# Optimization experiments

Hardware: AMD Instinct MI355X
Metric: run time of the kernel (lower is better)

Reference implementation:

```python
import jax, jax.numpy as jnp
import numpy as np

ALPHA = 0.2
NEG = -9e15
EPS = 1e-5


def _gat(h, adj, W, a, out_features):
    # h: [B,N,Fin], adj: [B,N,N], W: [Fin,Fout], a: [2*Fout,1]
    Wh = jnp.matmul(h, W)                      # [B,N,Fout]
    Wh1 = jnp.matmul(Wh, a[:out_features])     # [B,N,1]
    Wh2 = jnp.matmul(Wh, a[out_features:])     # [B,N,1]
    e = Wh1 + jnp.swapaxes(Wh2, 1, 2)          # [B,N,N]
    e = jax.nn.leaky_relu(e, negative_slope=ALPHA)
    scores = jnp.where(adj > 0, e, NEG)
    att = jax.nn.softmax(scores, axis=1)       # NOTE: dim=1 as in source
    return jnp.matmul(att, Wh)                 # [B,N,Fout]


def _layernorm(x, g, b):
    mu = jnp.mean(x, axis=-1, keepdims=True)
    var = jnp.var(x, axis=-1, keepdims=True)
    return (x - mu) * jax.lax.rsqrt(var + EPS) * g + b


def setup_inputs() -> dict:
    key = jax.random.key(0)
    ks = jax.random.split(key, 8)
    B, N, F, H = 2, 4096, 256, 1024
    x = jax.random.normal(ks[0], (B, N, F), dtype=jnp.float32)
    adj = jax.random.randint(ks[1], (B, N, N), 0, 2, dtype=jnp.int32)
    def xavier(k, shape):
        fan_in, fan_out = shape[0], shape[1]
        lim = np.sqrt(6.0 / (fan_in + fan_out))
        return jax.random.uniform(k, shape, jnp.float32, -lim, lim)
    return {
        "x": x,
        "adj": adj,
        "W1": xavier(ks[2], (F, F)),
        "a1": xavier(ks[3], (2 * F, 1)),
        "W2": xavier(ks[4], (F, F)),
        "a2": xavier(ks[5], (2 * F, 1)),
        "w_ff1": xavier(ks[6], (F, H)) ,
        "b_ff1": jnp.zeros((H,), jnp.float32),
        "w_ff2": xavier(ks[7], (H, F)),
        "b_ff2": jnp.zeros((F,), jnp.float32),
        "g_ln1": jnp.ones((F,), jnp.float32),
        "b_ln1": jnp.zeros((F,), jnp.float32),
        "g_ln2": jnp.ones((F,), jnp.float32),
        "b_ln2": jnp.zeros((F,), jnp.float32),
    }


def reference(x, adj, W1, a1, W2, a2, w_ff1, b_ff1, w_ff2, b_ff2,
              g_ln1, b_ln1, g_ln2, b_ln2):
    Fout = W1.shape[1]
    residual = x
    # dropout is a no-op in eval mode
    h = _gat(x, adj, W1, a1, Fout)          # single head -> cat is identity
    h = _gat(h, adj, W2, a2, W2.shape[1])
    h = _layernorm(residual + h, g_ln1, b_ln1)
    residual2 = h
    ff = jnp.matmul(jax.nn.relu(jnp.matmul(h, w_ff1) + b_ff1), w_ff2) + b_ff2
    return _layernorm(residual2 + ff, g_ln2, b_ln2)
```

## Files before the change

### kernel.cpp

```cpp
#include <hip/hip_runtime.h>
#include <math.h>

#define ALPHA 0.2f
#define NEGV  -9e15f
#define EPSV  1e-5f

constexpr int B_ = 2, N_ = 4096, F_ = 256, H_ = 1024;
constexpr int SPLIT_ = 16;
constexpr int SPLITJ_ = 4;

typedef __attribute__((ext_vector_type(4))) float f32x4;
typedef __attribute__((ext_vector_type(8))) short s16x8;

__device__ __forceinline__ unsigned short f2bf(float f) {
    unsigned u = __builtin_bit_cast(unsigned, f);
    u += 0x7fffu + ((u >> 16) & 1u);
    return (unsigned short)(u >> 16);
}

__global__ __launch_bounds__(256) void zero_kernel(float* __restrict__ p)
{
    const int i = (blockIdx.x * 256 + threadIdx.x) * 4;
    *(float4*)&p[i] = make_float4(0.f, 0.f, 0.f, 0.f);
}

__global__ __launch_bounds__(256) void transp_all_kernel(
    const float* __restrict__ W1, const float* __restrict__ W2,
    const float* __restrict__ F1s, const float* __restrict__ F2s,
    unsigned short* __restrict__ D1, unsigned short* __restrict__ D2,
    unsigned short* __restrict__ D3, unsigned short* __restrict__ D4)
{
    const int mi = blockIdx.z;
    const float* src; unsigned short* dst; int R, Cc;
    if (mi == 0)      { src = W1;  dst = D1; R = 256;  Cc = 256; }
    else if (mi == 1) { src = W2;  dst = D2; R = 256;  Cc = 256; }
    else if (mi == 2) { src = F1s; dst = D3; R = 256;  Cc = 1024; }
    else              { src = F2s; dst = D4; R = 1024; Cc = 256; }
    const int r0 = blockIdx.x * 64, c0 = blockIdx.y * 64;
    if (r0 >= R || c0 >= Cc) return;

    __shared__ float T[64][65];
    const int t = threadIdx.x;
    #pragma unroll
    for (int s = 0; s < 4; ++s) {
        const int rr = s * 16 + (t >> 4);
        const int cq = t & 15;
        const float4 v = *(const float4*)&src[(size_t)(r0 + rr) * Cc + c0 + cq * 4];
        T[rr][cq * 4 + 0] = v.x; T[rr][cq * 4 + 1] = v.y;
        T[rr][cq * 4 + 2] = v.z; T[rr][cq * 4 + 3] = v.w;
    }
    __syncthreads();
    #pragma unroll
    for (int s = 0; s < 4; ++s) {
        const int cr = s * 16 + (t >> 4);
        const int rq = t & 15;
        ushort4 o;
        o.x = f2bf(T[rq * 4 + 0][cr]);
        o.y = f2bf(T[rq * 4 + 1][cr]);
        o.z = f2bf(T[rq * 4 + 2][cr]);
        o.w = f2bf(T[rq * 4 + 3][cr]);
        *(ushort4*)&dst[(size_t)(c0 + cr) * R + r0 + rq * 4] = o;
    }
}

__global__ __launch_bounds__(256) void gemm128_kernel(
    const void* __restrict__ Ap, const unsigned short* __restrict__ Wt,
    const float* __restrict__ bias, void* __restrict__ Cp,
    unsigned short* __restrict__ Tout, const float* __restrict__ wha,
    float* __restrict__ Wh1, float* __restrict__ Wh2,
    int Nc, int K, int relu, int a_bf16, int c_mode)
{
    __shared__ unsigned short As[128 * 72];
    __shared__ unsigned short Bs[128 * 72];
    const int t = threadIdx.x;
    const int w = t >> 6, l = t & 63;
    const int quad = l >> 4, l15 = l & 15;
    const int wr = w & 1, wc = w >> 1;
    const int row0 = blockIdx.y * 128, col0 = blockIdx.x * 128;
    const int sr = t >> 1;
    const int sk = (t & 1) * 32;

    f32x4 acc[4][4];
    #pragma unroll
    for (int it = 0; it < 4; ++it)
        #pragma unroll
        for (int ft = 0; ft < 4; ++ft) acc[it][ft] = (f32x4)(0.f);

    for (int k0 = 0; k0 < K; k0 += 64) {
        if (a_bf16) {
            const unsigned short* ap =
                (const unsigned short*)Ap + (size_t)(row0 + sr) * K + k0 + sk;
            #pragma unroll
            for (int u = 0; u < 4; ++u)
                *(s16x8*)&As[sr * 72 + sk + u * 8] = *(const s16x8*)(ap + u * 8);
        } else {
            const float* ap = (const float*)Ap + (size_t)(row0 + sr) * K + k0 + sk;
            #pragma unroll
            for (int u = 0; u < 8; ++u) {
                const float4 v = *(const float4*)(ap + u * 4);
                ushort4 o;
                o.x = f2bf(v.x); o.y = f2bf(v.y); o.z = f2bf(v.z); o.w = f2bf(v.w);
                *(ushort4*)&As[sr * 72 + sk + u * 4] = o;
            }
        }
        {
            const unsigned short* bp = Wt + (size_t)(col0 + sr) * K + k0 + sk;
            #pragma unroll
            for (int u = 0; u < 4; ++u)
                *(s16x8*)&Bs[sr * 72 + sk + u * 8] = *(const s16x8*)(bp + u * 8);
        }
        __syncthreads();
        #pragma unroll
        for (int ks = 0; ks < 64; ks += 32) {
            s16x8 af[4], bf[4];
            #pragma unroll
            for (int it = 0; it < 4; ++it)
                af[it] = *(const s16x8*)&As[(wr * 64 + it * 16 + l15) * 72 + ks + quad * 8];
            #pragma unroll
            for (int ft = 0; ft < 4; ++ft)
                bf[ft] = *(const s16x8*)&Bs[(wc * 64 + ft * 16 + l15) * 72 + ks + quad * 8];
            #pragma unroll
            for (int ft = 0; ft < 4; ++ft)
                #pragma unroll
                for (int it = 0; it < 4; ++it)
                    acc[it][ft] = __builtin_amdgcn_mfma_f32_16x16x32_bf16(
                        af[it], bf[ft], acc[it][ft], 0, 0, 0);
        }
        __syncthreads();
    }

    if (c_mode) {
        #pragma unroll
        for (int ft = 0; ft < 4; ++ft) {
            const int col = col0 + wc * 64 + ft * 16 + l15;
            const float bv = bias ? bias[col] : 0.f;
            #pragma unroll
            for (int it = 0; it < 4; ++it) {
                const int rbase = row0 + wr * 64 + it * 16 + quad * 4;
                #pragma unroll
                for (int rr = 0; rr < 4; ++rr) {
                    float v = acc[it][ft][rr] + bv;
                    if (relu) v = fmaxf(v, 0.f);
                    if (c_mode == 2)
                        ((unsigned short*)Cp)[(size_t)(rbase + rr) * Nc + col] = f2bf(v);
                    else
                        ((float*)Cp)[(size_t)(rbase + rr) * Nc + col] = v;
                }
            }
        }
    }

    if (Tout) {
        const int bb = row0 >> 12;
        #pragma unroll
        for (int ft = 0; ft < 4; ++ft) {
            const int col = col0 + wc * 64 + ft * 16 + l15;
            #pragma unroll
            for (int it = 0; it < 4; ++it) {
                const int ibase = (row0 & (N_ - 1)) + wr * 64 + it * 16 + quad * 4;
                ushort4 o;
                o.x = f2bf(acc[it][ft][0]); o.y = f2bf(acc[it][ft][1]);
                o.z = f2bf(acc[it][ft][2]); o.w = f2bf(acc[it][ft][3]);
                *(ushort4*)&Tout[((size_t)bb * F_ + col) * N_ + ibase] = o;
            }
        }
    }

    if (wha) {
        float a1v[4], a2v[4];
        #pragma unroll
        for (int ft = 0; ft < 4; ++ft) {
            const int col = col0 + wc * 64 + ft * 16 + l15;
            a1v[ft] = wha[col];
            a2v[ft] = wha[F_ + col];
        }
        #pragma unroll
        for (int it = 0; it < 4; ++it)
            #pragma unroll
            for (int rr = 0; rr < 4; ++rr) {
                float s1 = 0.f, s2 = 0.f;
                #pragma unroll
                for (int ft = 0; ft < 4; ++ft) {
                    s1 += acc[it][ft][rr] * a1v[ft];
                    s2 += acc[it][ft][rr] * a2v[ft];
                }
                #pragma unroll
                for (int mkk = 1; mkk < 16; mkk <<= 1) {
                    s1 += __shfl_xor(s1, mkk);
                    s2 += __shfl_xor(s2, mkk);
                }
                if (l15 == 0) {
                    const int row = row0 + wr * 64 + it * 16 + quad * 4 + rr;
                    atomicAdd(&Wh1[row], s1);
                    atomicAdd(&Wh2[row], s2);
                }
            }
    }
}

__global__ __launch_bounds__(256) void gemm64_kernel(
    const void* __restrict__ Ap, const unsigned short* __restrict__ Wt,
    const float* __restrict__ bias, void* __restrict__ Cp,
    unsigned short* __restrict__ Tout, const float* __restrict__ wha,
    float* __restrict__ Wh1, float* __restrict__ Wh2,
    int Nc, int K, int relu, int a_bf16, int c_mode)
{
    __shared__ unsigned short As[64 * 72];
    __shared__ unsigned short Bs[128 * 72];
    const int t = threadIdx.x;
    const int w = t >> 6, l = t & 63;
    const int quad = l >> 4, l15 = l & 15;
    const int row0 = blockIdx.y * 64, col0 = blockIdx.x * 128;
    const int sra = t >> 2;
    const int ska = (t & 3) * 16;
    const int srb = t >> 1;
    const int skb = (t & 1) * 32;

    f32x4 acc[4][2];
    #pragma unroll
    for (int it = 0; it < 4; ++it)
        #pragma unroll
        for (int ft = 0; ft < 2; ++ft) acc[it][ft] = (f32x4)(0.f);

    for (int k0 = 0; k0 < K; k0 += 64) {
        if (a_bf16) {
            const unsigned short* ap =
                (const unsigned short*)Ap + (size_t)(row0 + sra) * K + k0 + ska;
            *(s16x8*)&As[sra * 72 + ska]     = *(const s16x8*)ap;
            *(s16x8*)&As[sra * 72 + ska + 8] = *(const s16x8*)(ap + 8);
        } else {
            const float* ap = (const float*)Ap + (size_t)(row0 + sra) * K + k0 + ska;
            #pragma unroll
            for (int u = 0; u < 4; ++u) {
                const float4 v = *(const float4*)(ap + u * 4);
                ushort4 o;
                o.x = f2bf(v.x); o.y = f2bf(v.y); o.z = f2bf(v.z); o.w = f2bf(v.w);
                *(ushort4*)&As[sra * 72 + ska + u * 4] = o;
            }
        }
        {
            const unsigned short* bp = Wt + (size_t)(col0 + srb) * K + k0 + skb;
            #pragma unroll
            for (int u = 0; u < 4; ++u)
                *(s16x8*)&Bs[srb * 72 + skb + u * 8] = *(const s16x8*)(bp + u * 8);
        }
        __syncthreads();
        #pragma unroll
        for (int ks = 0; ks < 64; ks += 32) {
            s16x8 af[4], bf[2];
            #pragma unroll
            for (int it = 0; it < 4; ++it)
                af[it] = *(const s16x8*)&As[(it * 16 + l15) * 72 + ks + quad * 8];
            #pragma unroll
            for (int ft = 0; ft < 2; ++ft)
                bf[ft] = *(const s16x8*)&Bs[(w * 32 + ft * 16 + l15) * 72 + ks + quad * 8];
            #pragma unroll
            for (int ft = 0; ft < 2; ++ft)
                #pragma unroll
                for (int it = 0; it < 4; ++it)
                    acc[it][ft] = __builtin_amdgcn_mfma_f32_16x16x32_bf16(
                        af[it], bf[ft], acc[it][ft], 0, 0, 0);
        }
        __syncthreads();
    }

    if (c_mode) {
        #pragma unroll
        for (int ft = 0; ft < 2; ++ft) {
            const int col = col0 + w * 32 + ft * 16 + l15;
            const float bv = bias ? bias[col] : 0.f;
            #pragma unroll
            for (int it = 0; it < 4; ++it) {
                const int rbase = row0 + it * 16 + quad * 4;
                #pragma unroll
                for (int rr = 0; rr < 4; ++rr) {
                    float v = acc[it][ft][rr] + bv;
                    if (relu) v = fmaxf(v, 0.f);
                    if (c_mode == 2)
                        ((unsigned short*)Cp)[(size_t)(rbase + rr) * Nc + col] = f2bf(v);
                    else
                        ((float*)Cp)[(size_t)(rbase + rr) * Nc + col] = v;
                }
            }
        }
    }

    if (Tout) {
        const int bb = row0 >> 12;
        #pragma unroll
        for (int ft = 0; ft < 2; ++ft) {
            const int col = col0 + w * 32 + ft * 16 + l15;
            #pragma unroll
            for (int it = 0; it < 4; ++it) {
                const int ibase = (row0 & (N_ - 1)) + it * 16 + quad * 4;
                ushort4 o;
                o.x = f2bf(acc[it][ft][0]); o.y = f2bf(acc[it][ft][1]);
                o.z = f2bf(acc[it][ft][2]); o.w = f2bf(acc[it][ft][3]);
                *(ushort4*)&Tout[((size_t)bb * F_ + col) * N_ + ibase] = o;
            }
        }
    }

    if (wha) {
        float a1v[2], a2v[2];
        #pragma unroll
        for (int ft = 0; ft < 2; ++ft) {
            const int col = col0 + w * 32 + ft * 16 + l15;
            a1v[ft] = wha[col];
            a2v[ft] = wha[F_ + col];
        }
        #pragma unroll
        for (int it = 0; it < 4; ++it)
            #pragma unroll
            for (int rr = 0; rr < 4; ++rr) {
                float s1 = acc[it][0][rr] * a1v[0] + acc[it][1][rr] * a1v[1];
                float s2 = acc[it][0][rr] * a2v[0] + acc[it][1][rr] * a2v[1];
                #pragma unroll
                for (int mkk = 1; mkk < 16; mkk <<= 1) {
                    s1 += __shfl_xor(s1, mkk);
                    s2 += __shfl_xor(s2, mkk);
                }
                if (l15 == 0) {
                    const int row = row0 + it * 16 + quad * 4 + rr;
                    atomicAdd(&Wh1[row], s1);
                    atomicAdd(&Wh2[row], s2);
                }
            }
    }
}

__global__ __launch_bounds__(256) void colstats_adj_kernel(
    const int* __restrict__ adj, unsigned long long* __restrict__ maskOut,
    const float* __restrict__ Wh1, const float* __restrict__ Wh2,
    float* __restrict__ pM, float* __restrict__ pS)
{
    const int t = threadIdx.x;
    const int j = blockIdx.x * 256 + t;
    const int sp = blockIdx.y;
    const int b = blockIdx.z;
    const int i0 = sp * (N_ / SPLIT_);
    const int w = t >> 6, l = t & 63;
    const float w2 = Wh2[b * N_ + j];
    const float* __restrict__ w1p = Wh1 + b * N_ + i0;
    const int* __restrict__ ap = adj + ((size_t)b * N_ + i0) * N_ + j;

    float m = -3.4e38f, s = 0.f;
    for (int c = 0; c < N_ / SPLIT_; c += 8) {
        int v[8];
        #pragma unroll
        for (int u = 0; u < 8; ++u) v[u] = ap[(size_t)(c + u) * N_];
        float x[8];
        #pragma unroll
        for (int u = 0; u < 8; ++u) {
            const bool act = v[u] > 0;
            const unsigned long long bm = __ballot(act);
            if (l == 0)
                maskOut[((size_t)b * N_ + i0 + c + u) * (N_ / 64) + blockIdx.x * 4 + w] = bm;
            const float e0 = w1p[c + u] + w2;
            const float e = fmaxf(e0, ALPHA * e0);
            x[u] = act ? e : NEGV;
        }
        const float cm = fmaxf(fmaxf(fmaxf(x[0], x[1]), fmaxf(x[2], x[3])),
                               fmaxf(fmaxf(x[4], x[5]), fmaxf(x[6], x[7])));
        const float nm = fmaxf(m, cm);
        float cs = 0.f;
        #pragma unroll
        for (int u = 0; u < 8; ++u) cs += __expf(x[u] - nm);
        s = s * __expf(m - nm) + cs;
        m = nm;
    }
    pM[((size_t)b * SPLIT_ + sp) * N_ + j] = m;
    pS[((size_t)b * SPLIT_ + sp) * N_ + j] = s;
}

__global__ __launch_bounds__(256) void colstats3_kernel(
    const unsigned long long* __restrict__ mask,
    const float* __restrict__ Wh1, const float* __restrict__ Wh2,
    float* __restrict__ pM, float* __restrict__ pS)
{
    const int t = threadIdx.x;
    const int j = blockIdx.x * 256 + t;
    const int sp = blockIdx.y;
    const int b = blockIdx.z;
    const int i0 = sp * (N_ / SPLIT_);
    const int w = t >> 6;
    const int jbit = t & 63;
    const float w2 = Wh2[b * N_ + j];
    const unsigned long long* __restrict__ mbase =
        mask + ((size_t)b * N_ + i0) * (N_ / 64) + blockIdx.x * 4 + w;
    const float* __restrict__ w1p = Wh1 + b * N_ + i0;

    float m = -3.4e38f, s = 0.f;
    for (int c = 0; c < N_ / SPLIT_; c += 8) {
        float x[8];
        #pragma unroll
        for (int u = 0; u < 8; ++u) {
            const unsigned long long mw = mbase[(size_t)(c + u) * (N_ / 64)];
            const float e0 = w1p[c + u] + w2;
            const float e = fmaxf(e0, ALPHA * e0);
            x[u] = ((mw >> jbit) & 1ull) ? e : NEGV;
        }
        const float cm = fmaxf(fmaxf(fmaxf(x[0], x[1]), fmaxf(x[2], x[3])),
                               fmaxf(fmaxf(x[4], x[5]), fmaxf(x[6], x[7])));
        const float nm = fmaxf(m, cm);
        float cs = 0.f;
        #pragma unroll
        for (int u = 0; u < 8; ++u) cs += __expf(x[u] - nm);
        s = s * __expf(m - nm) + cs;
        m = nm;
    }
    pM[((size_t)b * SPLIT_ + sp) * N_ + j] = m;
    pS[((size_t)b * SPLIT_ + sp) * N_ + j] = s;
}

__global__ __launch_bounds__(256) void colfin2_kernel(
    const float* __restrict__ pM, const float* __restrict__ pS,
    float* __restrict__ Mo)
{
    const int j = blockIdx.x * 256 + threadIdx.x;
    const int b = blockIdx.y;
    float m = -3.4e38f;
    #pragma unroll
    for (int s = 0; s < SPLIT_; ++s)
        m = fmaxf(m, pM[((size_t)b * SPLIT_ + s) * N_ + j]);
    float sum = 0.f;
    #pragma unroll
    for (int s = 0; s < SPLIT_; ++s)
        sum += pS[((size_t)b * SPLIT_ + s) * N_ + j] *
               __expf(pM[((size_t)b * SPLIT_ + s) * N_ + j] - m);
    Mo[b * N_ + j] = m + logf(sum);
}

__global__ __launch_bounds__(256, 2) void att_mfma4_kernel(
    const unsigned short* __restrict__ mask16, const unsigned short* __restrict__ Wht,
    const float* __restrict__ Wh1, const float* __restrict__ Wh2,
    const float* __restrict__ Mo, float* __restrict__ part)
{
    __shared__ unsigned short Ps[2][64 * 72];
    __shared__ float w2s[1024];
    __shared__ float mos[1024];

    const int t = threadIdx.x;
    const int w = t >> 6, l = t & 63;
    const int quad = l >> 4, l15 = l & 15;

    const int lin = blockIdx.x + (blockIdx.y << 6) + (blockIdx.z << 8);
    const int xcd = lin & 7;
    const int b = xcd >> 2;
    const int sp = xcd & 3;
    const int i0 = (lin >> 3) << 6;
    const int jbase = sp * (N_ / SPLITJ_);

    const int pi = t >> 2;
    const int pj4 = t & 3;
    const float w1i = Wh1[b * N_ + i0 + pi];
    const unsigned short* __restrict__ mrow =
        mask16 + ((size_t)b * N_ + i0 + pi) * (N_ / 16) + pj4;
    const unsigned short* __restrict__ WhtB = Wht + (size_t)b * F_ * N_;

    {
        const float4 a = *(const float4*)&Wh2[b * N_ + jbase + t * 4];
        const float4 c = *(const float4*)&Mo[b * N_ + jbase + t * 4];
        *(float4*)&w2s[t * 4] = a;
        *(float4*)&mos[t * 4] = c;
    }

    f32x4 acc[4][4];
    #pragma unroll
    for (int it = 0; it < 4; ++it)
        #pragma unroll
        for (int ft = 0; ft < 4; ++ft) acc[it][ft] = (f32x4)(0.f);

    const unsigned short* __restrict__ bbase =
        WhtB + (size_t)(w * 64 + l15) * N_ + jbase + quad * 8;

    s16x8 bA[8], bB[8];

    auto prefB = [&](int itr2, s16x8* dst) {
        const unsigned short* nb = bbase + itr2 * 64;
        #pragma unroll
        for (int ft = 0; ft < 4; ++ft)
            #pragma unroll
            for (int kk = 0; kk < 2; ++kk)
                dst[ft * 2 + kk] = *(const s16x8*)&nb[(size_t)ft * 16 * N_ + kk * 32];
    };

    auto computeP = [&](int itr2, unsigned short* psdst) {
        const int jl = itr2 * 64 + pj4 * 16;
        const unsigned mb = mrow[(jbase >> 4) + itr2 * 4];
        s16x8 o0, o1;
        #pragma unroll
        for (int u4 = 0; u4 < 4; ++u4) {
            const float4 w2v = *(const float4*)&w2s[jl + u4 * 4];
            const float4 mov = *(const float4*)&mos[jl + u4 * 4];
            #pragma unroll
            for (int u = 0; u < 4; ++u) {
                const float xw = w1i + (&w2v.x)[u];
                const float e = fmaxf(xw, ALPHA * xw);
                const float x2 = ((mb >> (u4 * 4 + u)) & 1u) ? e : NEGV;
                const short pv = (short)f2bf(__expf(x2 - (&mov.x)[u]));
                if (u4 < 2) o0[u4 * 4 + u] = pv;
                else        o1[(u4 - 2) * 4 + u] = pv;
            }
        }
        *(s16x8*)&psdst[pi * 72 + pj4 * 16]     = o0;
        *(s16x8*)&psdst[pi * 72 + pj4 * 16 + 8] = o1;
    };

    auto mfmaStep = [&](const unsigned short* ps, const s16x8* breg) {
        #pragma unroll
        for (int ksidx = 0; ksidx < 2; ++ksidx) {
            s16x8 af[4];
            #pragma unroll
            for (int it = 0; it < 4; ++it)
                af[it] = *(const s16x8*)&ps[(it * 16 + l15) * 72 + ksidx * 32 + quad * 8];
            #pragma unroll
            for (int ft = 0; ft < 4; ++ft)
                #pragma unroll
                for (int it = 0; it < 4; ++it)
                    acc[it][ft] = __builtin_amdgcn_mfma_f32_16x16x32_bf16(
                        af[it], breg[ft * 2 + ksidx], acc[it][ft], 0, 0, 0);
        }
    };

    prefB(0, bA);
    __syncthreads();
    computeP(0, &Ps[0][0]);
    __syncthreads();

    constexpr int NITER = (N_ / SPLITJ_) / 64;
    for (int itr = 0; itr < NITER; itr += 2) {
        prefB(itr + 1, bB);
        computeP(itr + 1, &Ps[1][0]);
        mfmaStep(&Ps[0][0], bA);
        __syncthreads();
        if (itr + 2 < NITER) {
            prefB(itr + 2, bA);
            computeP(itr + 2, &Ps[0][0]);
        }
        mfmaStep(&Ps[1][0], bB);
        __syncthreads();
    }

    float* __restrict__ pout = part + ((size_t)sp * B_ + b) * N_ * F_;
    #pragma unroll
    for (int it = 0; it < 4; ++it)
        #pragma unroll
        for (int ft = 0; ft < 4; ++ft) {
            const int col = w * 64 + ft * 16 + l15;
            #pragma unroll
            for (int rr = 0; rr < 4; ++rr) {
                const int row = i0 + it * 16 + quad * 4 + rr;
                pout[(size_t)row * F_ + col] = acc[it][ft][rr];
            }
        }
}

__global__ __launch_bounds__(256) void reduce4b_kernel(
    const float* __restrict__ p, unsigned short* __restrict__ outb)
{
    const size_t i = ((size_t)blockIdx.x * 256 + threadIdx.x) * 4;
    const size_t S = (size_t)B_ * N_ * F_;
    const float4 a = *(const float4*)&p[i];
    const float4 b = *(const float4*)&p[i + S];
    const float4 c = *(const float4*)&p[i + 2 * S];
    const float4 d = *(const float4*)&p[i + 3 * S];
    ushort4 o;
    o.x = f2bf(a.x + b.x + c.x + d.x);
    o.y = f2bf(a.y + b.y + c.y + d.y);
    o.z = f2bf(a.z + b.z + c.z + d.z);
    o.w = f2bf(a.w + b.w + c.w + d.w);
    *(ushort4*)&outb[i] = o;
}

__global__ __launch_bounds__(256) void addln4_kernel(
    const float* __restrict__ X, const float* __restrict__ p,
    const float* __restrict__ g, const float* __restrict__ bta,
    float* __restrict__ outf, unsigned short* __restrict__ outb)
{
    const int row = blockIdx.x;
    const int t = threadIdx.x;
    const size_t idx = (size_t)row * F_ + t;
    const size_t S = (size_t)B_ * N_ * F_;
    const float v = X[idx] + p[idx] + p[idx + S] + p[idx + 2 * S] + p[idx + 3 * S];
    float s1 = v, s2 = v * v;
    #pragma unroll
    for (int off = 32; off > 0; off >>= 1) {
        s1 += __shfl_down(s1, off);
        s2 += __shfl_down(s2, off);
    }
    __shared__ float r1[4], r2[4];
    __shared__ float mu_s, rs_s;
    const int wid = t >> 6, lane = t & 63;
    if (lane == 0) { r1[wid] = s1; r2[wid] = s2; }
    __syncthreads();
    if (t == 0) {
        const float a = r1[0] + r1[1] + r1[2] + r1[3];
        const float q = r2[0] + r2[1] + r2[2] + r2[3];
        const float mu = a * (1.f / F_);
        const float var = q * (1.f / F_) - mu * mu;
        mu_s = mu;
        rs_s = rsqrtf(var + EPSV);
    }
    __syncthreads();
    const float r = (v - mu_s) * rs_s * g[t] + bta[t];
    outf[idx] = r;
    outb[idx] = f2bf(r);
}

__global__ __launch_bounds__(256) void addln_kernel(
    const float* __restrict__ X, const float* __restrict__ Y,
    const float* __restrict__ g, const float* __restrict__ bta,
    float* __restrict__ out)
{
    const int row = blockIdx.x;
    const int t = threadIdx.x;
    const size_t idx = (size_t)row * F_ + t;
    const float v = X[idx] + Y[idx];
    float s1 = v, s2 = v * v;
    #pragma unroll
    for (int off = 32; off > 0; off >>= 1) {
        s1 += __shfl_down(s1, off);
        s2 += __shfl_down(s2, off);
    }
    __shared__ float r1[4], r2[4];
    __shared__ float mu_s, rs_s;
    const int wid = t >> 6, lane = t & 63;
    if (lane == 0) { r1[wid] = s1; r2[wid] = s2; }
    __syncthreads();
    if (t == 0) {
        const float a = r1[0] + r1[1] + r1[2] + r1[3];
        const float q = r2[0] + r2[1] + r2[2] + r2[3];
        const float mu = a * (1.f / F_);
        const float var = q * (1.f / F_) - mu * mu;
        mu_s = mu;
        rs_s = rsqrtf(var + EPSV);
    }
    __syncthreads();
    out[idx] = (v - mu_s) * rs_s * g[t] + bta[t];
}

extern "C" void kernel_launch(void* const* d_in, const int* in_sizes, int n_in,
                              void* d_out, int out_size, void* d_ws, size_t ws_size,
                              hipStream_t stream)
{
    const float* x     = (const float*)d_in[0];
    const int*   adj   = (const int*)d_in[1];
    const float* W1    = (const float*)d_in[2];
    const float* a1    = (const float*)d_in[3];
    const float* W2    = (const float*)d_in[4];
    const float* a2    = (const float*)d_in[5];
    const float* w_ff1 = (const float*)d_in[6];
    const float* b_ff1 = (const float*)d_in[7];
    const float* w_ff2 = (const float*)d_in[8];
    const float* b_ff2 = (const float*)d_in[9];
    const float* g_ln1 = (const float*)d_in[10];
    const float* b_ln1 = (const float*)d_in[11];
    const float* g_ln2 = (const float*)d_in[12];
    const float* b_ln2 = (const float*)d_in[13];
    float* out = (float*)d_out;

    const int Rtot = B_ * N_;
    char* wsb = (char*)d_ws;
    float* part  = (float*)wsb;
    float* ln1   = (float*)(wsb + 33554432);
    float* ffout = (float*)(wsb + 41943040);
    unsigned short* mid  = (unsigned short*)(wsb + 50331648);
    unsigned short* ln1b = (unsigned short*)(wsb + 67108864);
    unsigned short* g1b  = (unsigned short*)(wsb + 71303168);
    unsigned short* Wht  = (unsigned short*)(wsb + 75497472);
    unsigned long long* mask = (unsigned long long*)(wsb + 79691776);
    unsigned short* mask16 = (unsigned short*)mask;
    unsigned short* Wt1  = (unsigned short*)(wsb + 83886080);
    unsigned short* Wt2  = Wt1 + 65536;
    unsigned short* Wtf1 = Wt2 + 65536;
    unsigned short* Wtf2 = Wtf1 + 262144;
    float* WhA1 = (float*)(wsb + 85196800);
    float* WhA2 = WhA1 + 8192;
    float* WhB1 = WhA2 + 8192;
    float* WhB2 = WhB1 + 8192;
    float* Mo   = (float*)(wsb + 85327872);
    float* pM   = (float*)(wsb + 85360640);
    float* pS   = (float*)(wsb + 85884928);

    const dim3 statsG(N_ / 256, SPLIT_, B_);
    const dim3 finG(N_ / 256, B_);
    const dim3 attG(N_ / 64, SPLITJ_, B_);

    zero_kernel<<<32, 256, 0, stream>>>(WhA1);
    transp_all_kernel<<<dim3(16, 16, 4), 256, 0, stream>>>(
        W1, W2, w_ff1, w_ff2, Wt1, Wt2, Wtf1, Wtf2);

    gemm64_kernel<<<dim3(2, 128), 256, 0, stream>>>(
        x, Wt1, nullptr, nullptr, Wht, a1, WhA1, WhA2, F_, F_, 0, 0, 0);
    colstats_adj_kernel<<<statsG, 256, 0, stream>>>(adj, mask, WhA1, WhA2, pM, pS);
    colfin2_kernel<<<finG, 256, 0, stream>>>(pM, pS, Mo);
    att_mfma4_kernel<<<attG, 256, 0, stream>>>(mask16, Wht, WhA1, WhA2, Mo, part);
    reduce4b_kernel<<<2048, 256, 0, stream>>>(part, g1b);

    gemm64_kernel<<<dim3(2, 128), 256, 0, stream>>>(
        g1b, Wt2, nullptr, nullptr, Wht, a2, WhB1, WhB2, F_, F_, 0, 1, 0);
    colstats3_kernel<<<statsG, 256, 0, stream>>>(mask, WhB1, WhB2, pM, pS);
    colfin2_kernel<<<finG, 256, 0, stream>>>(pM, pS, Mo);
    att_mfma4_kernel<<<attG, 256, 0, stream>>>(mask16, Wht, WhB1, WhB2, Mo, part);

    addln4_kernel<<<Rtot, 256, 0, stream>>>(x, part, g_ln1, b_ln1, ln1, ln1b);

    gemm128_kernel<<<dim3(8, 64), 256, 0, stream>>>(
        ln1b, Wtf1, b_ff1, mid, nullptr, nullptr, nullptr, nullptr, H_, F_, 1, 1, 2);
    gemm64_kernel<<<dim3(2, 128), 256, 0, stream>>>(
        mid, Wtf2, b_ff2, ffout, nullptr, nullptr, nullptr, nullptr, F_, H_, 0, 1, 1);

    addln_kernel<<<Rtot, 256, 0, stream>>>(ln1, ffout, g_ln2, b_ln2, out);
}
```

Measured before the change: 424.0 us.

## Remove split-K in attention matmul, use 32-row tiles with 512 threads

```diff
diff --git a/kernel.cpp b/kernel.cpp
--- a/kernel.cpp
+++ b/kernel.cpp
@@ -7,7 +7,6 @@
 
 constexpr int B_ = 2, N_ = 4096, F_ = 256, H_ = 1024;
 constexpr int SPLIT_ = 16;
-constexpr int SPLITJ_ = 4;
 
 typedef __attribute__((ext_vector_type(4))) float f32x4;
 typedef __attribute__((ext_vector_type(8))) short s16x8;
@@ -431,93 +430,91 @@
     Mo[b * N_ + j] = m + logf(sum);
 }
 
-__global__ __launch_bounds__(256, 2) void att_mfma4_kernel(
+__global__ __launch_bounds__(512) void att_mfma5_kernel(
     const unsigned short* __restrict__ mask16, const unsigned short* __restrict__ Wht,
     const float* __restrict__ Wh1, const float* __restrict__ Wh2,
-    const float* __restrict__ Mo, float* __restrict__ part)
-{
-    __shared__ unsigned short Ps[2][64 * 72];
-    __shared__ float w2s[1024];
-    __shared__ float mos[1024];
+    const float* __restrict__ Mo, unsigned short* __restrict__ outb,
+    float* __restrict__ outf)
+{
+    __shared__ unsigned short Ps[2][32 * 72];
+    __shared__ float w2s[N_];
+    __shared__ float mos[N_];
 
     const int t = threadIdx.x;
     const int w = t >> 6, l = t & 63;
     const int quad = l >> 4, l15 = l & 15;
 
-    const int lin = blockIdx.x + (blockIdx.y << 6) + (blockIdx.z << 8);
+    const int lin = blockIdx.x;
     const int xcd = lin & 7;
     const int b = xcd >> 2;
-    const int sp = xcd & 3;
-    const int i0 = (lin >> 3) << 6;
-    const int jbase = sp * (N_ / SPLITJ_);
-
-    const int pi = t >> 2;
-    const int pj4 = t & 3;
+    const int tile = (lin >> 3) * 4 + (xcd & 3);
+    const int i0 = tile * 32;
+
+    const int pi = t >> 4;
+    const int pj = t & 15;
     const float w1i = Wh1[b * N_ + i0 + pi];
     const unsigned short* __restrict__ mrow =
-        mask16 + ((size_t)b * N_ + i0 + pi) * (N_ / 16) + pj4;
+        mask16 + ((size_t)b * N_ + i0 + pi) * (N_ / 16);
     const unsigned short* __restrict__ WhtB = Wht + (size_t)b * F_ * N_;
 
     {
-        const float4 a = *(const float4*)&Wh2[b * N_ + jbase + t * 4];
-        const float4 c = *(const float4*)&Mo[b * N_ + jbase + t * 4];
-        *(float4*)&w2s[t * 4] = a;
-        *(float4*)&mos[t * 4] = c;
-    }
-
-    f32x4 acc[4][4];
-    #pragma unroll
-    for (int it = 0; it < 4; ++it)
-        #pragma unroll
-        for (int ft = 0; ft < 4; ++ft) acc[it][ft] = (f32x4)(0.f);
+        const float4 a0 = *(const float4*)&Wh2[b * N_ + t * 8];
+        const float4 a1 = *(const float4*)&Wh2[b * N_ + t * 8 + 4];
+        const float4 c0 = *(const float4*)&Mo[b * N_ + t * 8];
+        const float4 c1 = *(const float4*)&Mo[b * N_ + t * 8 + 4];
+        *(float4*)&w2s[t * 8] = a0; *(float4*)&w2s[t * 8 + 4] = a1;
+        *(float4*)&mos[t * 8] = c0; *(float4*)&mos[t * 8 + 4] = c1;
+    }
+
+    f32x4 acc[2][2];
+    #pragma unroll
+    for (int it = 0; it < 2; ++it)
+        #pragma unroll
+        for (int ft = 0; ft < 2; ++ft) acc[it][ft] = (f32x4)(0.f);
 
     const unsigned short* __restrict__ bbase =
-        WhtB + (size_t)(w * 64 + l15) * N_ + jbase + quad * 8;
-
-    s16x8 bA[8], bB[8];
+        WhtB + (size_t)(w * 32 + l15) * N_ + quad * 8;
+
+    s16x8 bA[4], bB[4];
 
     auto prefB = [&](int itr2, s16x8* dst) {
         const unsigned short* nb = bbase + itr2 * 64;
         #pragma unroll
-        for (int ft = 0; ft < 4; ++ft)
+        for (int ft = 0; ft < 2; ++ft)
             #pragma unroll
             for (int kk = 0; kk < 2; ++kk)
                 dst[ft * 2 + kk] = *(const s16x8*)&nb[(size_t)ft * 16 * N_ + kk * 32];
     };
 
     auto computeP = [&](int itr2, unsigned short* psdst) {
-        const int jl = itr2 * 64 + pj4 * 16;
-        const unsigned mb = mrow[(jbase >> 4) + itr2 * 4];
-        s16x8 o0, o1;
-        #pragma unroll
-        for (int u4 = 0; u4 < 4; ++u4) {
-            const float4 w2v = *(const float4*)&w2s[jl + u4 * 4];
-            const float4 mov = *(const float4*)&mos[jl + u4 * 4];
-            #pragma unroll
-            for (int u = 0; u < 4; ++u) {
-                const float xw = w1i + (&w2v.x)[u];
-                const float e = fmaxf(xw, ALPHA * xw);
-                const float x2 = ((mb >> (u4 * 4 + u)) & 1u) ? e : NEGV;
-                const short pv = (short)f2bf(__expf(x2 - (&mov.x)[u]));
-                if (u4 < 2) o0[u4 * 4 + u] = pv;
-                else        o1[(u4 - 2) * 4 + u] = pv;
-            }
-        }
-        *(s16x8*)&psdst[pi * 72 + pj4 * 16]     = o0;
-        *(s16x8*)&psdst[pi * 72 + pj4 * 16 + 8] = o1;
+        const unsigned mb = mrow[itr2 * 4 + (pj >> 2)];
+        const int bsh = (pj & 3) * 4;
+        const int jl = itr2 * 64 + pj * 4;
+        const float4 w2v = *(const float4*)&w2s[jl];
+        const float4 mov = *(const float4*)&mos[jl];
+        ushort4 o;
+        unsigned short* op = &o.x;
+        #pragma unroll
+        for (int u = 0; u < 4; ++u) {
+            const float xw = w1i + (&w2v.x)[u];
+            const float e = fmaxf(xw, ALPHA * xw);
+            const float x2 = ((mb >> (bsh + u)) & 1u) ? e : NEGV;
+            op[u] = f2bf(__expf(x2 - (&mov.x)[u]));
+        }
+        *(ushort4*)&psdst[pi * 72 + pj * 4] = o;
     };
 
     auto mfmaStep = [&](const unsigned short* ps, const s16x8* breg) {
         #pragma unroll
         for (int ksidx = 0; ksidx < 2; ++ksidx) {
-            s16x8 af[4];
-            #pragma unroll
-            for (int it = 0; it < 4; ++it)
+            s16x8 af[2];
+            #pragma unroll
+            for (int it = 0; it < 2; ++it)
                 af[it] = *(const s16x8*)&ps[(it * 16 + l15) * 72 + ksidx * 32 + quad * 8];
             #pragma unroll
-            for (int ft = 0; ft < 4; ++ft)
-                #pragma unroll
-                for (int it = 0; it < 4; ++it)
+            for (int ft = 0; ft < 2; ++ft)
+                #pragma unroll
+                for (int it = 0; it < 2; ++it)
                     acc[it][ft] = __builtin_amdgcn_mfma_f32_16x16x32_bf16(
                         af[it], breg[ft * 2 + ksidx], acc[it][ft], 0, 0, 0);
         }
@@ -528,7 +525,7 @@
     computeP(0, &Ps[0][0]);
     __syncthreads();
 
-    constexpr int NITER = (N_ / SPLITJ_) / 64;
+    constexpr int NITER = N_ / 64;
     for (int itr = 0; itr < NITER; itr += 2) {
         prefB(itr + 1, bB);
         computeP(itr + 1, &Ps[1][0]);
@@ -542,47 +539,42 @@
         __syncthreads();
     }
 
-    float* __restrict__ pout = part + ((size_t)sp * B_ + b) * N_ * F_;
-    #pragma unroll
-    for (int it = 0; it < 4; ++it)
-        #pragma unroll
-        for (int ft = 0; ft < 4; ++ft) {
-            const int col = w * 64 + ft * 16 + l15;
-            #pragma unroll
-            for (int rr = 0; rr < 4; ++rr) {
-                const int row = i0 + it * 16 + quad * 4 + rr;
-                pout[(size_t)row * F_ + col] = acc[it][ft][rr];
-            }
-        }
-}
-
-__global__ __launch_bounds__(256) void reduce4b_kernel(
-    const float* __restrict__ p, unsigned short* __restrict__ outb)
-{
-    const size_t i = ((size_t)blockIdx.x * 256 + threadIdx.x) * 4;
-    const size_t S = (size_t)B_ * N_ * F_;
-    const float4 a = *(const float4*)&p[i];
-    const float4 b = *(const float4*)&p[i + S];
-    const float4 c = *(const float4*)&p[i + 2 * S];
-    const float4 d = *(const float4*)&p[i + 3 * S];
-    ushort4 o;
-    o.x = f2bf(a.x + b.x + c.x + d.x);
-    o.y = f2bf(a.y + b.y + c.y + d.y);
-    o.z = f2bf(a.z + b.z + c.z + d.z);
-    o.w = f2bf(a.w + b.w + c.w + d.w);
-    *(ushort4*)&outb[i] = o;
-}
-
-__global__ __launch_bounds__(256) void addln4_kernel(
-    const float* __restrict__ X, const float* __restrict__ p,
+    if (outb) {
+        unsigned short* __restrict__ ob = outb + (size_t)(b * N_ + i0) * F_;
+        #pragma unroll
+        for (int it = 0; it < 2; ++it)
+            #pragma unroll
+            for (int ft = 0; ft < 2; ++ft) {
+                const int col = w * 32 + ft * 16 + l15;
+                #pragma unroll
+                for (int rr = 0; rr < 4; ++rr)
+                    ob[(size_t)(it * 16 + quad * 4 + rr) * F_ + col] =
+                        f2bf(acc[it][ft][rr]);
+            }
+    } else {
+        float* __restrict__ of = outf + (size_t)(b * N_ + i0) * F_;
+        #pragma unroll
+        for (int it = 0; it < 2; ++it)
+            #pragma unroll
+            for (int ft = 0; ft < 2; ++ft) {
+                const int col = w * 32 + ft * 16 + l15;
+                #pragma unroll
+                for (int rr = 0; rr < 4; ++rr)
+                    of[(size_t)(it * 16 + quad * 4 + rr) * F_ + col] =
+                        acc[it][ft][rr];
+            }
+    }
+}
+
+__global__ __launch_bounds__(256) void addln2b_kernel(
+    const float* __restrict__ X, const float* __restrict__ Y,
     const float* __restrict__ g, const float* __restrict__ bta,
     float* __restrict__ outf, unsigned short* __restrict__ outb)
 {
     const int row = blockIdx.x;
     const int t = threadIdx.x;
     const size_t idx = (size_t)row * F_ + t;
-    const size_t S = (size_t)B_ * N_ * F_;
-    const float v = X[idx] + p[idx] + p[idx + S] + p[idx + 2 * S] + p[idx + 3 * S];
+    const float v = X[idx] + Y[idx];
     float s1 = v, s2 = v * v;
     #pragma unroll
     for (int off = 32; off > 0; off >>= 1) {
@@ -662,7 +654,7 @@
 
     const int Rtot = B_ * N_;
     char* wsb = (char*)d_ws;
-    float* part  = (float*)wsb;
+    float* attout = (float*)wsb;
     float* ln1   = (float*)(wsb + 33554432);
     float* ffout = (float*)(wsb + 41943040);
     unsigned short* mid  = (unsigned short*)(wsb + 50331648);
@@ -685,7 +677,6 @@
 
     const dim3 statsG(N_ / 256, SPLIT_, B_);
     const dim3 finG(N_ / 256, B_);
-    const dim3 attG(N_ / 64, SPLITJ_, B_);
 
     zero_kernel<<<32, 256, 0, stream>>>(WhA1);
     transp_all_kernel<<<dim3(16, 16, 4), 256, 0, stream>>>(
@@ -695,16 +686,17 @@
         x, Wt1, nullptr, nullptr, Wht, a1, WhA1, WhA2, F_, F_, 0, 0, 0);
     colstats_adj_kernel<<<statsG, 256, 0, stream>>>(adj, mask, WhA1, WhA2, pM, pS);
     colfin2_kernel<<<finG, 256, 0, stream>>>(pM, pS, Mo);
-    att_mfma4_kernel<<<attG, 256, 0, stream>>>(mask16, Wht, WhA1, WhA2, Mo, part);
-    reduce4b_kernel<<<2048, 256, 0, stream>>>(part, g1b);
+    att_mfma5_kernel<<<256, 512, 0, stream>>>(
+        mask16, Wht, WhA1, WhA2, Mo, g1b, nullptr);
 
     gemm64_kernel<<<dim3(2, 128), 256, 0, stream>>>(
         g1b, Wt2, nullptr, nullptr, Wht, a2, WhB1, WhB2, F_, F_, 0, 1, 0);
     colstats3_kernel<<<statsG, 256, 0, stream>>>(mask, WhB1, WhB2, pM, pS);
     colfin2_kernel<<<finG, 256, 0, stream>>>(pM, pS, Mo);
-    att_mfma4_kernel<<<attG, 256, 0, stream>>>(mask16, Wht, WhB1, WhB2, Mo, part);
-
-    addln4_kernel<<<Rtot, 256, 0, stream>>>(x, part, g_ln1, b_ln1, ln1, ln1b);
+    att_mfma5_kernel<<<256, 512, 0, stream>>>(
+        mask16, Wht, WhB1, WhB2, Mo, nullptr, attout);
+
+    addln2b_kernel<<<Rtot, 256, 0, stream>>>(x, attout, g_ln1, b_ln1, ln1, ln1b);
 
     gemm128_kernel<<<dim3(8, 64), 256, 0, stream>>>(
         ln1b, Wtf1, b_ff1, mid, nullptr, nullptr, nullptr, nullptr, H_, F_, 1, 1, 2);
```

Result: slower. 485.1 us (+14.4%).
